# Kernel tuning notes

Hardware: AMD Instinct MI355X
Metric: run time of the kernel (lower is better)

The kernel has to match this reference:

```python
import jax, jax.numpy as jnp
import numpy as np

ATOM_K = 10
VOX_K = 15
HEADS = 4
HEAD_DIM = 32
N_BLOCKS = 4
BLOCK_DEPTH = 2


def _pairwise_sqdist(a, b):
    # a: [Na,3], b: [Nb,3] -> [Na,Nb]
    return jnp.sum(a * a, 1)[:, None] + jnp.sum(b * b, 1)[None, :] - 2.0 * (a @ b.T)


def knn(src_pos, dst_pos, k):
    # for each dst point, k nearest src points; returns (dst_idx, src_idx), each [Nd*k]
    d2 = _pairwise_sqdist(dst_pos, src_pos)
    _, idx = jax.lax.top_k(-d2, k)
    dst = jnp.repeat(jnp.arange(dst_pos.shape[0]), k)
    return dst, idx.reshape(-1)


def knn_graph(pos, k):
    # k nearest neighbors excluding self; returns (src=neighbor, dst=center)
    n = pos.shape[0]
    d2 = _pairwise_sqdist(pos, pos) + jnp.eye(n, dtype=pos.dtype) * 1e10
    _, idx = jax.lax.top_k(-d2, k)
    dst = jnp.repeat(jnp.arange(n), k)
    return idx.reshape(-1), dst


def edge_weights(i0, i1, h_a, pos_a, h_b, pos_b, w1, b1, w2, b2):
    # MLP([2*A+1, 8, 1]) on concat(h_a[i0], h_b[i1], dist) -> scalar per edge
    d = jnp.sqrt(jnp.sum((pos_a[i0] - pos_b[i1]) ** 2, -1, keepdims=True) + 1e-12)
    feat = jnp.concatenate([h_a[i0], h_b[i1], d], -1)
    return (jax.nn.relu(feat @ w1 + b1) @ w2 + b2)[:, 0]


def attn_layer(h, src, dst, ew, wq_l, wk_l, wv_l, n):
    # edge-weighted multi-head graph attention with segment softmax over dst
    q = (h @ wq_l).reshape(n, HEADS, HEAD_DIM)
    k = (h @ wk_l).reshape(n, HEADS, HEAD_DIM)
    v = (h @ wv_l).reshape(n, HEADS, HEAD_DIM)
    logits = jnp.sum(q[dst] * k[src], -1) / jnp.sqrt(jnp.float32(HEAD_DIM)) + ew[:, None]  # [E,H]
    m = jax.ops.segment_max(logits, dst, num_segments=n)
    z = jnp.exp(logits - m[dst])
    s = jax.ops.segment_sum(z, dst, num_segments=n)
    alpha = z / (s[dst] + 1e-9)
    out = jax.ops.segment_sum(alpha[:, :, None] * v[src], dst, num_segments=n)
    return out.reshape(n, HEADS * HEAD_DIM)


def layer_norm(x, g, b):
    mu = jnp.mean(x, -1, keepdims=True)
    var = jnp.var(x, -1, keepdims=True)
    return (x - mu) * jax.lax.rsqrt(var + 1e-5) * g + b


def setup_inputs() -> dict:
    Na, Nv, F, A, OUT = 8192, 4096, 64, 128, 128
    L = N_BLOCKS * BLOCK_DEPTH
    key = jax.random.key(0)
    ks = jax.random.split(key, 20)
    p = lambda k, shape, s=0.05: jax.random.normal(k, shape, jnp.float32) * s
    return {
        'atom_x': jax.random.normal(ks[0], (Na, F), jnp.float32),
        'atom_pos': jax.random.normal(ks[1], (Na, 3), jnp.float32) * 10.0,
        'vox_x': jax.random.normal(ks[2], (Nv, F), jnp.float32),
        'vox_pos': jax.random.normal(ks[3], (Nv, 3), jnp.float32) * 10.0,
        'w_atom_in': p(ks[4], (F, A)), 'b_atom_in': jnp.zeros((A,), jnp.float32),
        'w_vox_in': p(ks[5], (F, A)), 'b_vox_in': jnp.zeros((A,), jnp.float32),
        'aa_w1': p(ks[6], (2 * A + 1, 8)), 'aa_b1': jnp.zeros((8,), jnp.float32),
        'aa_w2': p(ks[7], (8, 1)), 'aa_b2': jnp.zeros((1,), jnp.float32),
        'av_w1': p(ks[8], (2 * A + 1, 8)), 'av_b1': jnp.zeros((8,), jnp.float32),
        'av_w2': p(ks[9], (8, 1)), 'av_b2': jnp.zeros((1,), jnp.float32),
        'vv_w1': p(ks[10], (2 * A + 1, 8)), 'vv_b1': jnp.zeros((8,), jnp.float32),
        'vv_w2': p(ks[11], (8, 1)), 'vv_b2': jnp.zeros((1,), jnp.float32),
        'wq': p(ks[12], (L, A, A)), 'wk': p(ks[13], (L, A, A)), 'wv': p(ks[14], (L, A, A)),
        'ln_g': jnp.ones((L, A), jnp.float32), 'ln_b': jnp.zeros((L, A), jnp.float32),
        'w_o1': p(ks[15], ((N_BLOCKS + 1) * A, A)), 'b_o1': jnp.zeros((A,), jnp.float32),
        'w_o2': p(ks[16], (A, OUT)), 'b_o2': jnp.zeros((OUT,), jnp.float32),
    }


def reference(atom_x, atom_pos, vox_x, vox_pos, w_atom_in, b_atom_in, w_vox_in, b_vox_in,
              aa_w1, aa_b1, aa_w2, aa_b2, av_w1, av_b1, av_w2, av_b2, vv_w1, vv_b1, vv_w2, vv_b2,
              wq, wk, wv, ln_g, ln_b, w_o1, b_o1, w_o2, b_o2):
    Na, Nv = atom_x.shape[0], vox_x.shape[0]
    N = Na + Nv
    atom_h0 = atom_x @ w_atom_in + b_atom_in
    vox_h0 = vox_x @ w_vox_in + b_vox_in

    # multi-scale KNN graph construction
    aa_src, aa_dst = knn_graph(atom_pos, ATOM_K)
    aa_ew = edge_weights(aa_src, aa_dst, atom_h0, atom_pos, atom_h0, atom_pos, aa_w1, aa_b1, aa_w2, aa_b2)
    av_vox, av_atom = knn(atom_pos, vox_pos, VOX_K)  # dst=vox, src=atom
    av_ew = edge_weights(av_vox, av_atom, vox_h0, vox_pos, atom_h0, atom_pos, av_w1, av_b1, av_w2, av_b2)
    vv_src, vv_dst = knn_graph(vox_pos, VOX_K)
    vv_ew = edge_weights(vv_src, vv_dst, vox_h0, vox_pos, vox_h0, vox_pos, vv_w1, vv_b1, vv_w2, vv_b2)

    # combined atom|vox graph (vox nodes offset by Na)
    src = jnp.concatenate([aa_src, av_atom, vv_src + Na])
    dst = jnp.concatenate([aa_dst, av_vox + Na, vv_dst + Na])
    ew = jnp.concatenate([aa_ew, av_ew, vv_ew])
    h = jnp.concatenate([atom_h0, vox_h0], 0)

    block_outs = []
    for b_i in range(N_BLOCKS):
        for l in range(BLOCK_DEPTH):
            li = b_i * BLOCK_DEPTH + l
            h = layer_norm(h + attn_layer(h, src, dst, ew, wq[li], wk[li], wv[li], N), ln_g[li], ln_b[li])
        block_outs.append(h[Na:])

    feat = jnp.concatenate([vox_h0] + block_outs, -1)  # [Nv, (blocks+1)*A]
    return jax.nn.relu(feat @ w_o1 + b_o1) @ w_o2 + b_o2
```

## Files before the change

kernel.cpp:

```cpp
#include <hip/hip_runtime.h>
#include <hip/hip_bf16.h>

#define PE_NA 8192
#define PE_NV 4096
#define PE_NN (PE_NA+PE_NV)
#define PE_FA 128
#define PE_FIN 64
#define PE_KAA 10
#define PE_KAV 15
#define PE_KVV 15
#define PE_EAA (PE_NA*PE_KAA)
#define PE_EAV (PE_NV*PE_KAV)
#define PE_EVV (PE_NV*PE_KVV)
#define PE_ETOT (PE_EAA+PE_EAV+PE_EVV)
#define PE_KNN_TILE 1024
#define PE_KNN_BLOCKS (PE_NA/4 + PE_NV/4 + PE_NV/4)
#define PE_P1A 0
#define PE_P2A 65536
#define PE_P2AV 131072
#define PE_P1AV 196608
#define PE_P1V 229376
#define PE_P2V 262144
#define PE_PTOT 294912
#define PE_PRE_BLOCKS (PE_PTOT/256)
#define PE_WT_ELEMS (8*3*128*128)
#define PE_WT_BLOCKS (PE_WT_ELEMS/256)

typedef __hip_bfloat16 bf16;
typedef __attribute__((ext_vector_type(4))) float f32x4;
typedef __attribute__((ext_vector_type(4))) unsigned int u32x4;
typedef __attribute__((ext_vector_type(8))) short s16x8;
union pe_frag { u32x4 u; s16x8 s; };

__device__ __forceinline__ float pe_b2f(bf16 x){ return __bfloat162float(x); }

__device__ __forceinline__ float pe_u2f(unsigned short u){ return __uint_as_float(((unsigned)u) << 16); }
__device__ __forceinline__ unsigned short pe_f2u(float f){
  unsigned u = __float_as_uint(f);
  u = u + 0x7FFFu + ((u >> 16) & 1u);
  return (unsigned short)(u >> 16);
}

__global__ __launch_bounds__(1024) void pe_probe_kernel(const unsigned short* __restrict__ buf, int n,
                                                        int* __restrict__ flag){
  __shared__ int red[16];
  int t = threadIdx.x;
  int cnt = 0;
  for (int i = t; i < n; i += 1024){
    unsigned u = buf[i];
    unsigned e = (u >> 7) & 0xFF;
    if (u == 0u || (e >= 100u && e <= 150u)) cnt++;
  }
  #pragma unroll
  for (int off = 32; off > 0; off >>= 1) cnt += __shfl_xor(cnt, off);
  if ((t & 63) == 0) red[t >> 6] = cnt;
  __syncthreads();
  if (t == 0){
    int s = 0;
    #pragma unroll
    for (int i = 0; i < 16; i++) s += red[i];
    flag[0] = (s > (n * 9) / 10) ? 0 : 1;
  }
}

struct PeConv {
  const void* src[29];
  long long dstOff[29];
  int n[29];
  int blk0[30];
};
__global__ __launch_bounds__(256) void pe_convall_kernel(PeConv a, float* __restrict__ wsbase,
                                                         const int* __restrict__ flag){
  int b = blockIdx.x;
  int s = 0;
  while (s < 28 && b >= a.blk0[s+1]) s++;
  int idx = (b - a.blk0[s])*256 + threadIdx.x;
  if (idx >= a.n[s]) return;
  float* dst = wsbase + a.dstOff[s];
  if (flag[0]) dst[idx] = ((const float*)a.src[s])[idx];
  else         dst[idx] = pe_b2f(((const bf16*)a.src[s])[idx]);
}

__global__ __launch_bounds__(256) void ProteinEncoder_558345749244_kernel(bf16* __restrict__ out, int n){
  int idx = blockIdx.x*256 + threadIdx.x;
  if (idx < n) out[idx] = __float2bfloat16(0.123f);
}

__global__ __launch_bounds__(256) void pe_packproj_kernel(
    const float* __restrict__ ax, const float* __restrict__ wai, const float* __restrict__ bai,
    const float* __restrict__ vx, const float* __restrict__ wvi, const float* __restrict__ bvi,
    const float* __restrict__ apos, const float* __restrict__ vpos,
    const float* __restrict__ wq, const float* __restrict__ wk, const float* __restrict__ wv,
    float* __restrict__ h, float* __restrict__ voxh0,
    float4* __restrict__ apos4, float4* __restrict__ vpos4,
    unsigned short* __restrict__ wtb){
  int b = blockIdx.x;
  const int NBA = (PE_NA*PE_FA)/256;
  const int NBV = (PE_NV*PE_FA)/256;
  const int NBP = (PE_NN + 255)/256;
  if (b < NBA){
    int idx = b*256 + threadIdx.x;
    int row = idx >> 7, col = idx & 127;
    const float* xr = ax + row*PE_FIN;
    float acc = bai[col];
    #pragma unroll 8
    for (int k2 = 0; k2 < PE_FIN; k2++) acc += xr[k2] * wai[k2*PE_FA + col];
    h[idx] = acc;
  } else if (b < NBA + NBV){
    int idx = (b - NBA)*256 + threadIdx.x;
    int row = idx >> 7, col = idx & 127;
    const float* xr = vx + row*PE_FIN;
    float acc = bvi[col];
    #pragma unroll 8
    for (int k2 = 0; k2 < PE_FIN; k2++) acc += xr[k2] * wvi[k2*PE_FA + col];
    h[(size_t)PE_NA*PE_FA + idx] = acc;
    voxh0[idx] = acc;
  } else if (b < NBA + NBV + NBP){
    int idx = (b - NBA - NBV)*256 + threadIdx.x;
    if (idx < PE_NA){
      float bx = apos[idx*3+0], by = apos[idx*3+1], bz = apos[idx*3+2];
      apos4[idx] = make_float4(bx, by, bz, (bx*bx + by*by) + bz*bz);
    } else if (idx < PE_NA + PE_NV){
      int j = idx - PE_NA;
      float bx = vpos[j*3+0], by = vpos[j*3+1], bz = vpos[j*3+2];
      vpos4[j] = make_float4(bx, by, bz, (bx*bx + by*by) + bz*bz);
    }
  } else {
    int g = (b - NBA - NBV - NBP)*256 + threadIdx.x;
    int c = g >> 14;
    int r = g & 16383;
    int n = r >> 7, k = r & 127;
    int li = c / 3, mat = c - li*3;
    const float* wsrc = (mat == 0) ? wq : (mat == 1) ? wk : wv;
    wtb[g] = pe_f2u(wsrc[li*16384 + k*128 + n]);
  }
}

__device__ __forceinline__ float pe_unflip(unsigned th){
  return __uint_as_float(th ^ ((unsigned)(~((int)th >> 31)) | 0x80000000u));
}
__device__ __forceinline__ void pe_knn_insert(unsigned long long mask, float d2, int j,
                                              int self, int K, int lane,
                                              unsigned long long &slot, float &thr_f){
  while (mask){
    int l = __ffsll((long long)mask) - 1;
    mask &= mask - 1;
    float dl = __shfl(d2, l, 64);
    int jl = __shfl(j, l, 64);
    if (jl == self) continue;
    unsigned u = __float_as_uint(dl);
    u ^= (unsigned)(((int)u >> 31) | 0x80000000);
    unsigned long long k = ((unsigned long long)u << 32) | (unsigned)jl;
    unsigned long long skm1 = __shfl(slot, K-1, 64);
    if (k < skm1){
      unsigned long long up = __shfl_up(slot, 1, 64);
      slot = (slot < k) ? slot : ((lane == 0 || up < k) ? k : up);
      thr_f = pe_unflip((unsigned)(__shfl(slot, K-1, 64) >> 32));
    }
  }
}

__global__ __launch_bounds__(256) void pe_knn3_kernel(const float4* __restrict__ apos4,
                                                      const float4* __restrict__ vpos4,
                                                      int* __restrict__ es,
                                                      const float* __restrict__ h,
                                                      const float* __restrict__ aw1,
                                                      const float* __restrict__ vw1,
                                                      const float* __restrict__ ww1,
                                                      float* __restrict__ Pall){
  __shared__ float4 s_tile[PE_KNN_TILE];
  int b = blockIdx.x;
  if (b >= PE_KNN_BLOCKS){
    int g = (b - PE_KNN_BLOCKS)*256 + threadIdx.x;
    const float* w1; const float* hb; int n; int half;
    if (g < PE_P2A)       { w1 = aw1; hb = h;                        n = g >> 3;               half = 0; }
    else if (g < PE_P2AV) { w1 = aw1; hb = h;                        n = (g - PE_P2A) >> 3;    half = 1; }
    else if (g < PE_P1AV) { w1 = vw1; hb = h;                        n = (g - PE_P2AV) >> 3;   half = 1; }
    else if (g < PE_P1V)  { w1 = vw1; hb = h + (size_t)PE_NA*PE_FA;  n = (g - PE_P1AV) >> 3;   half = 0; }
    else if (g < PE_P2V)  { w1 = ww1; hb = h + (size_t)PE_NA*PE_FA;  n = (g - PE_P1V) >> 3;    half = 0; }
    else                  { w1 = ww1; hb = h + (size_t)PE_NA*PE_FA;  n = (g - PE_P2V) >> 3;    half = 1; }
    int j = g & 7;
    const float* hr = hb + n*PE_FA;
    const float* wr = w1 + half*128*8 + j;
    float acc = 0.f;
    #pragma unroll 8
    for (int f = 0; f < 128; f++) acc += hr[f] * wr[f*8];
    Pall[g] = acc;
    return;
  }
  const float4 *dpos, *spos; int Ns, K, excl, idx_off, nb; int* out;
  if (b < PE_NA/4){
    dpos = apos4; spos = apos4; Ns = PE_NA; K = PE_KAA; excl = 1; idx_off = 0;
    out = es; nb = b;
  } else if (b < PE_NA/4 + PE_NV/4){
    dpos = vpos4; spos = apos4; Ns = PE_NA; K = PE_KAV; excl = 0; idx_off = 0;
    out = es + PE_EAA; nb = b - PE_NA/4;
  } else {
    dpos = vpos4; spos = vpos4; Ns = PE_NV; K = PE_KVV; excl = 1; idx_off = PE_NA;
    out = es + PE_EAA + PE_EAV; nb = b - PE_NA/4 - PE_NV/4;
  }
  int lane = threadIdx.x & 63;
  int n = nb*4 + (threadIdx.x >> 6);
  float4 dp = dpos[n];
  float ax = dp.x, ay = dp.y, az = dp.z;
  int self = excl ? n : -1;
  unsigned long long slot;
  float thr_f;
  {
    float4 pp = spos[lane];
    float dt = (ax*pp.x + ay*pp.y) + az*pp.z;
    float d2 = __builtin_fmaf(-2.0f, dt, pp.w);
    unsigned u = __float_as_uint(d2);
    u ^= (unsigned)(((int)u >> 31) | 0x80000000);
    if (excl && lane == n) u = 0xffffffffu;
    unsigned long long key = ((unsigned long long)u << 32) | (unsigned)lane;
    #pragma unroll
    for (int kk = 2; kk <= 64; kk <<= 1){
      #pragma unroll
      for (int jj = kk >> 1; jj > 0; jj >>= 1){
        unsigned long long o = __shfl_xor(key, jj, 64);
        bool keepmin = (((lane & jj) == 0) == ((lane & kk) == 0));
        unsigned long long mn = (key < o) ? key : o;
        unsigned long long mx = (key < o) ? o : key;
        key = keepmin ? mn : mx;
      }
    }
    slot = key;
    thr_f = pe_unflip((unsigned)(__shfl(slot, K-1, 64) >> 32));
  }
  for (int base = 0; base < Ns; base += PE_KNN_TILE){
    __syncthreads();
    #pragma unroll
    for (int i = 0; i < PE_KNN_TILE/256; i++)
      s_tile[i*256 + threadIdx.x] = spos[base + i*256 + threadIdx.x];
    __syncthreads();
    int c = (base == 0) ? (lane + 64) : lane;
    for (; c + 192 < PE_KNN_TILE; c += 256){
      float4 p0 = s_tile[c];
      float4 p1 = s_tile[c + 64];
      float4 p2 = s_tile[c + 128];
      float4 p3 = s_tile[c + 192];
      float dt0 = (ax*p0.x + ay*p0.y) + az*p0.z;
      float dt1 = (ax*p1.x + ay*p1.y) + az*p1.z;
      float dt2 = (ax*p2.x + ay*p2.y) + az*p2.z;
      float dt3 = (ax*p3.x + ay*p3.y) + az*p3.z;
      float d20 = __builtin_fmaf(-2.0f, dt0, p0.w);
      float d21 = __builtin_fmaf(-2.0f, dt1, p1.w);
      float d22 = __builtin_fmaf(-2.0f, dt2, p2.w);
      float d23 = __builtin_fmaf(-2.0f, dt3, p3.w);
      unsigned long long m0 = __ballot(d20 <= thr_f);
      unsigned long long m1 = __ballot(d21 <= thr_f);
      unsigned long long m2 = __ballot(d22 <= thr_f);
      unsigned long long m3 = __ballot(d23 <= thr_f);
      if (m0) pe_knn_insert(m0, d20, base + c,       self, K, lane, slot, thr_f);
      if (m1) pe_knn_insert(m1, d21, base + c + 64,  self, K, lane, slot, thr_f);
      if (m2) pe_knn_insert(m2, d22, base + c + 128, self, K, lane, slot, thr_f);
      if (m3) pe_knn_insert(m3, d23, base + c + 192, self, K, lane, slot, thr_f);
    }
    for (; c + 64 < PE_KNN_TILE; c += 128){
      float4 p0 = s_tile[c];
      float4 p1 = s_tile[c + 64];
      float dt0 = (ax*p0.x + ay*p0.y) + az*p0.z;
      float dt1 = (ax*p1.x + ay*p1.y) + az*p1.z;
      float d20 = __builtin_fmaf(-2.0f, dt0, p0.w);
      float d21 = __builtin_fmaf(-2.0f, dt1, p1.w);
      unsigned long long m0 = __ballot(d20 <= thr_f);
      unsigned long long m1 = __ballot(d21 <= thr_f);
      if (m0) pe_knn_insert(m0, d20, base + c,      self, K, lane, slot, thr_f);
      if (m1) pe_knn_insert(m1, d21, base + c + 64, self, K, lane, slot, thr_f);
    }
    if (c < PE_KNN_TILE){
      float4 p0 = s_tile[c];
      float dt0 = (ax*p0.x + ay*p0.y) + az*p0.z;
      float d20 = __builtin_fmaf(-2.0f, dt0, p0.w);
      unsigned long long m0 = __ballot(d20 <= thr_f);
      if (m0) pe_knn_insert(m0, d20, base + c, self, K, lane, slot, thr_f);
    }
  }
  if (lane < K) out[n*K + lane] = (int)(unsigned)(slot & 0xffffffffu) + idx_off;
}

__global__ __launch_bounds__(256) void pe_edge3_kernel(
    const float4* __restrict__ apos4, const float4* __restrict__ vpos4,
    const int* __restrict__ es, const float* __restrict__ Pall,
    const float* __restrict__ aw1, const float* __restrict__ ab1,
    const float* __restrict__ aw2, const float* __restrict__ ab2,
    const float* __restrict__ vw1, const float* __restrict__ vb1,
    const float* __restrict__ vw2, const float* __restrict__ vb2,
    const float* __restrict__ ww1, const float* __restrict__ wb1,
    const float* __restrict__ ww2, const float* __restrict__ wb2,
    float* __restrict__ ewb){
  int e = blockIdx.x*256 + threadIdx.x;
  const float *w1r, *b1, *w2, *b2;
  long long offA, offB;
  float4 qa, qb;
  if (e < PE_EAA){
    int dst = e / PE_KAA;
    int src = es[e];
    offA = PE_P1A  + (long long)src*8;
    offB = PE_P2A  + (long long)dst*8;
    qa = apos4[src]; qb = apos4[dst];
    w1r = aw1 + 256*8; b1 = ab1; w2 = aw2; b2 = ab2;
  } else if (e < PE_EAA + PE_EAV){
    int e2 = e - PE_EAA;
    int dstv = e2 / PE_KAV;
    int srca = es[e];
    offA = PE_P1AV + (long long)dstv*8;
    offB = PE_P2AV + (long long)srca*8;
    qa = vpos4[dstv]; qb = apos4[srca];
    w1r = vw1 + 256*8; b1 = vb1; w2 = vw2; b2 = vb2;
  } else {
    int e2 = e - PE_EAA - PE_EAV;
    int dstv = e2 / PE_KVV;
    int srcv = es[e] - PE_NA;
    offA = PE_P1V  + (long long)srcv*8;
    offB = PE_P2V  + (long long)dstv*8;
    qa = vpos4[srcv]; qb = vpos4[dstv];
    w1r = ww1 + 256*8; b1 = wb1; w2 = ww2; b2 = wb2;
  }
  float dx = qa.x - qb.x, dy = qa.y - qb.y, dz = qa.z - qb.z;
  float d = sqrtf(((dx*dx + dy*dy) + dz*dz) + 1e-12f);
  float4 a0 = *(const float4*)(Pall + offA);
  float4 a1 = *(const float4*)(Pall + offA + 4);
  float4 c0 = *(const float4*)(Pall + offB);
  float4 c1 = *(const float4*)(Pall + offB + 4);
  float acc[8] = { a0.x + c0.x, a0.y + c0.y, a0.z + c0.z, a0.w + c0.w,
                   a1.x + c1.x, a1.y + c1.y, a1.z + c1.z, a1.w + c1.w };
  float o = b2[0];
  #pragma unroll
  for (int j = 0; j < 8; j++){
    float hj = acc[j] + d*w1r[j] + b1[j];
    if (hj > 0.f) o += hj * w2[j];
  }
  ewb[e] = o;
}

__global__ __launch_bounds__(256) void pe_qkv3_kernel(const float* __restrict__ H,
    const unsigned short* __restrict__ Wt,
    unsigned short* __restrict__ QKV){
  __shared__ __align__(16) unsigned Xs[2048];
  int t = threadIdx.x;
  int row0 = blockIdx.x * 32;
  #pragma unroll
  for (int i = 0; i < 8; i++){
    int idx32 = i*256 + t;
    int row = idx32 >> 6, c32 = idx32 & 63;
    const float* src = H + (size_t)(row0 + row)*PE_FA + c32*2;
    unsigned u = (unsigned)pe_f2u(src[0]) | ((unsigned)pe_f2u(src[1]) << 16);
    Xs[row*64 + (c32 ^ ((row & 7) << 2))] = u;
  }
  __syncthreads();
  int w = t >> 6, l = t & 63;
  int l15 = l & 15, lq = l >> 4;
  f32x4 acc[2][6];
  #pragma unroll
  for (int a = 0; a < 2; a++)
    #pragma unroll
    for (int bb = 0; bb < 6; bb++) acc[a][bb] = (f32x4){0.f, 0.f, 0.f, 0.f};
  #pragma unroll
  for (int ks = 0; ks < 4; ks++){
    pe_frag af[2];
    #pragma unroll
    for (int rt = 0; rt < 2; rt++){
      int row = rt*16 + l15;
      int c32 = (ks*16 + lq*4) ^ ((row & 7) << 2);
      af[rt].u = *(const u32x4*)&Xs[row*64 + c32];
    }
    #pragma unroll
    for (int nt = 0; nt < 6; nt++){
      int n = w*96 + nt*16 + l15;
      pe_frag bf_;
      bf_.u = *(const u32x4*)(Wt + (size_t)n*PE_FA + ks*32 + lq*8);
      #pragma unroll
      for (int rt = 0; rt < 2; rt++)
        acc[rt][nt] = __builtin_amdgcn_mfma_f32_16x16x32_bf16(af[rt].s, bf_.s, acc[rt][nt], 0, 0, 0);
    }
  }
  #pragma unroll
  for (int rt = 0; rt < 2; rt++){
    #pragma unroll
    for (int nt = 0; nt < 6; nt++){
      int n = w*96 + nt*16 + l15;
      int mat = n >> 7, col = n & 127;
      unsigned short* outp = QKV + (size_t)mat*PE_NN*PE_FA + col;
      int nodeb = row0 + rt*16 + lq*4;
      #pragma unroll
      for (int v = 0; v < 4; v++)
        outp[(size_t)(nodeb + v)*PE_FA] = pe_f2u(acc[rt][nt][v]);
    }
  }
}

template<int DEG>
__device__ __forceinline__ void pe_attn_node(int n, int lane, int esel, float ewsel,
    const unsigned* __restrict__ Qp, const unsigned* __restrict__ Kp, const unsigned* __restrict__ Vp,
    float* H, const float* __restrict__ lng, const float* __restrict__ lnb, float* bout){
  unsigned qu = Qp[n*64 + lane];
  float qx = pe_u2f((unsigned short)(qu & 0xffffu));
  float qy = pe_u2f((unsigned short)(qu >> 16));
  int srcs[DEG];
  #pragma unroll
  for (int e = 0; e < DEG; e++) srcs[e] = __shfl(esel, e, 64);
  const float inv = 0.17677669529663687f;
  float lg[DEG];
  #pragma unroll
  for (int e = 0; e < DEG; e++){
    unsigned ku = Kp[srcs[e]*64 + lane];
    float p = qx*pe_u2f((unsigned short)(ku & 0xffffu)) + qy*pe_u2f((unsigned short)(ku >> 16));
    #pragma unroll
    for (int off = 8; off > 0; off >>= 1) p += __shfl_xor(p, off);
    lg[e] = p*inv + __shfl(ewsel, e, 64);
  }
  float m = -1e30f;
  #pragma unroll
  for (int e = 0; e < DEG; e++) m = fmaxf(m, lg[e]);
  float ssum = 0.f;
  #pragma unroll
  for (int e = 0; e < DEG; e++){ float z = expf(lg[e] - m); ssum += z; lg[e] = z; }
  float rdn = 1.0f / (ssum + 1e-9f);
  float a0 = 0.f, a1 = 0.f;
  #pragma unroll
  for (int e = 0; e < DEG; e++){
    unsigned vu = Vp[srcs[e]*64 + lane];
    a0 += lg[e]*pe_u2f((unsigned short)(vu & 0xffffu));
    a1 += lg[e]*pe_u2f((unsigned short)(vu >> 16));
  }
  a0 *= rdn; a1 *= rdn;
  float2 hv = ((const float2*)H)[n*64 + lane];
  float x0 = hv.x + a0, x1 = hv.y + a1;
  float s = x0 + x1;
  #pragma unroll
  for (int off = 32; off > 0; off >>= 1) s += __shfl_xor(s, off);
  float mu = s * (1.f/128.f);
  float d0 = x0 - mu, d1 = x1 - mu;
  float vq = d0*d0 + d1*d1;
  #pragma unroll
  for (int off = 32; off > 0; off >>= 1) vq += __shfl_xor(vq, off);
  float var = vq * (1.f/128.f);
  float rs = 1.0f / sqrtf(var + 1e-5f);
  float2 lw = ((const float2*)lng)[lane];
  float2 lb = ((const float2*)lnb)[lane];
  float2 yv = make_float2(d0*rs*lw.x + lb.x, d1*rs*lw.y + lb.y);
  ((float2*)H)[n*64 + lane] = yv;
  if (bout != nullptr) ((float2*)bout)[(n - PE_NA)*64 + lane] = yv;
}

__global__ __launch_bounds__(128) void pe_attn_ln_kernel(const unsigned* __restrict__ Qp,
    const unsigned* __restrict__ Kp, const unsigned* __restrict__ Vp, float* H,
    const int* __restrict__ esrc, const float* __restrict__ eew,
    const float* __restrict__ lng, const float* __restrict__ lnb, float* bout){
  int w = threadIdx.x >> 6;
  int lane = threadIdx.x & 63;
  int n = blockIdx.x*2 + w;
  int esel = 0; float ewsel = 0.f;
  if (n < PE_NA){
    if (lane < PE_KAA){ int e = n*PE_KAA + lane; esel = esrc[e]; ewsel = eew[e]; }
    pe_attn_node<PE_KAA>(n, lane, esel, ewsel, Qp, Kp, Vp, H, lng, lnb, nullptr);
  } else {
    int j = n - PE_NA;
    if (lane < PE_KAV){ int e = PE_EAA + j*PE_KAV + lane; esel = esrc[e]; ewsel = eew[e]; }
    else if (lane < PE_KAV + PE_KVV){ int e = PE_EAA + PE_EAV + j*PE_KVV + (lane - PE_KAV); esel = esrc[e]; ewsel = eew[e]; }
    pe_attn_node<PE_KAV+PE_KVV>(n, lane, esel, ewsel, Qp, Kp, Vp, H, lng, lnb, bout);
  }
}

__global__ __launch_bounds__(256) void pe_final1_kernel(const float* __restrict__ voxh0, const float* __restrict__ bouts,
    const float* __restrict__ W, const float* __restrict__ B, float* __restrict__ hid){
  __shared__ float Xs[640][17];
  int t = threadIdx.x;
  int row0 = blockIdx.x * 16;
  for (int s = 0; s < 5; s++){
    const float* seg = (s == 0) ? voxh0 : (bouts + (size_t)(s-1)*PE_NV*PE_FA);
    #pragma unroll
    for (int i = 0; i < 8; i++){
      int idx = i*256 + t;
      int r = idx >> 7, k0 = idx & 127;
      Xs[s*128 + k0][r] = seg[(size_t)(row0 + r)*PE_FA + k0];
    }
  }
  __syncthreads();
  int col = t & 127;
  int rg = (t >> 7) * 8;
  float acc[8];
  #pragma unroll
  for (int i = 0; i < 8; i++) acc[i] = B[col];
  for (int k = 0; k < 640; k++){
    float w = W[k*PE_FA + col];
    #pragma unroll
    for (int i = 0; i < 8; i++) acc[i] += Xs[k][rg + i] * w;
  }
  #pragma unroll
  for (int i = 0; i < 8; i++)
    hid[(size_t)(row0 + rg + i)*PE_FA + col] = fmaxf(acc[i], 0.f);
}

__global__ __launch_bounds__(256) void pe_final2_kernel(const float* __restrict__ hid, const float* __restrict__ W,
    const float* __restrict__ B, void* __restrict__ outv, const int* __restrict__ flag){
  int idx = blockIdx.x*256 + threadIdx.x;
  int r = idx >> 7, c = idx & 127;
  float acc = B[c];
  const float* hr = hid + r*PE_FA;
  #pragma unroll 8
  for (int k2 = 0; k2 < 128; k2++) acc += hr[k2] * W[k2*PE_FA + c];
  if (flag[0]) ((float*)outv)[idx] = acc;
  else         ((bf16*)outv)[idx] = __float2bfloat16(acc);
}

extern "C" void kernel_launch(void* const* d_in, const int* in_sizes, int n_in,
                              void* d_out, int out_size, void* d_ws, size_t ws_size,
                              hipStream_t stream){
  (void)in_sizes; (void)n_in; (void)ws_size;

  float* ws = (float*)d_ws;
  int* flag = (int*)ws;
  float* p = ws + 4;
  auto A = [&](size_t n){ float* r = p; p += n; return r; };

  float* c_atom_x  = A(PE_NA*PE_FIN);
  float* c_atom_pos= A(PE_NA*3);
  float* c_vox_x   = A(PE_NV*PE_FIN);
  float* c_vox_pos = A(PE_NV*3);
  float* c_w_ai = A(PE_FIN*PE_FA); float* c_b_ai = A(PE_FA);
  float* c_w_vi = A(PE_FIN*PE_FA); float* c_b_vi = A(PE_FA);
  float* c_aa_w1 = A(257*8); float* c_aa_b1 = A(8); float* c_aa_w2 = A(8); float* c_aa_b2 = A(1);
  float* c_av_w1 = A(257*8); float* c_av_b1 = A(8); float* c_av_w2 = A(8); float* c_av_b2 = A(1);
  float* c_vv_w1 = A(257*8); float* c_vv_b1 = A(8); float* c_vv_w2 = A(8); float* c_vv_b2 = A(1);
  float* c_wq = A(8*PE_FA*PE_FA); float* c_wk = A(8*PE_FA*PE_FA); float* c_wv = A(8*PE_FA*PE_FA);
  float* c_lng = A(8*PE_FA); float* c_lnb = A(8*PE_FA);
  float* c_wo1 = A(5*PE_FA*PE_FA); float* c_bo1 = A(PE_FA);
  float* c_wo2 = A(PE_FA*PE_FA);   float* c_bo2 = A(PE_FA);

  float* h     = A((size_t)PE_NN*PE_FA);
  float* voxh0 = A((size_t)PE_NV*PE_FA);
  int*   es    = (int*)A(PE_ETOT);
  float* ewb   = A(PE_ETOT);
  float* bouts = A((size_t)4*PE_NV*PE_FA);
  float4* apos4 = (float4*)A((size_t)PE_NA*4);
  float4* vpos4 = (float4*)A((size_t)PE_NV*4);
  { uintptr_t up = (uintptr_t)p; up = (up + 15) & ~(uintptr_t)15; p = (float*)up; }
  float* Pall  = A(PE_PTOT);
  unsigned short* wtb = (unsigned short*)A(PE_WT_ELEMS/2);
  float* qkvb  = A((size_t)3*PE_NN*64);
  unsigned short* qkvb16 = (unsigned short*)qkvb;
  float* hid   = qkvb;

  pe_probe_kernel<<<1, 1024, 0, stream>>>((const unsigned short*)d_in[1], PE_NA*3, flag);

  const int nelem[29] = {
    PE_NA*PE_FIN, PE_NA*3, PE_NV*PE_FIN, PE_NV*3,
    PE_FIN*PE_FA, PE_FA, PE_FIN*PE_FA, PE_FA,
    257*8, 8, 8, 1,  257*8, 8, 8, 1,  257*8, 8, 8, 1,
    8*PE_FA*PE_FA, 8*PE_FA*PE_FA, 8*PE_FA*PE_FA,
    8*PE_FA, 8*PE_FA,
    5*PE_FA*PE_FA, PE_FA, PE_FA*PE_FA, PE_FA
  };
  float* cdst[29] = {
    c_atom_x, c_atom_pos, c_vox_x, c_vox_pos,
    c_w_ai, c_b_ai, c_w_vi, c_b_vi,
    c_aa_w1, c_aa_b1, c_aa_w2, c_aa_b2,
    c_av_w1, c_av_b1, c_av_w2, c_av_b2,
    c_vv_w1, c_vv_b1, c_vv_w2, c_vv_b2,
    c_wq, c_wk, c_wv, c_lng, c_lnb,
    c_wo1, c_bo1, c_wo2, c_bo2
  };
  PeConv pc;
  int bacc = 0;
  for (int i = 0; i < 29; i++){
    pc.src[i] = d_in[i];
    pc.n[i] = nelem[i];
    pc.dstOff[i] = (long long)(cdst[i] - ws);
    pc.blk0[i] = bacc;
    bacc += (nelem[i] + 255)/256;
  }
  pc.blk0[29] = bacc;
  pe_convall_kernel<<<bacc, 256, 0, stream>>>(pc, ws, flag);

  ProteinEncoder_558345749244_kernel<<<(out_size + 255)/256, 256, 0, stream>>>((bf16*)d_out, out_size);

  pe_packproj_kernel<<<(PE_NA*PE_FA)/256 + (PE_NV*PE_FA)/256 + (PE_NN + 255)/256 + PE_WT_BLOCKS,
                       256, 0, stream>>>(
      c_atom_x, c_w_ai, c_b_ai, c_vox_x, c_w_vi, c_b_vi, c_atom_pos, c_vox_pos,
      c_wq, c_wk, c_wv,
      h, voxh0, apos4, vpos4, wtb);

  pe_knn3_kernel<<<PE_KNN_BLOCKS + PE_PRE_BLOCKS, 256, 0, stream>>>(
      apos4, vpos4, es, h, c_aa_w1, c_av_w1, c_vv_w1, Pall);

  pe_edge3_kernel<<<PE_ETOT/256, 256, 0, stream>>>(
      apos4, vpos4, es, Pall,
      c_aa_w1, c_aa_b1, c_aa_w2, c_aa_b2,
      c_av_w1, c_av_b1, c_av_w2, c_av_b2,
      c_vv_w1, c_vv_b1, c_vv_w2, c_vv_b2,
      ewb);

  const unsigned* Qp = (const unsigned*)qkvb;
  const unsigned* Kp = Qp + (size_t)PE_NN*64;
  const unsigned* Vp = Kp + (size_t)PE_NN*64;
  for (int li = 0; li < 8; li++){
    pe_qkv3_kernel<<<PE_NN/32, 256, 0, stream>>>(h, wtb + (size_t)li*3*PE_FA*PE_FA, qkvb16);
    float* bo = (li & 1) ? (bouts + (size_t)(li >> 1)*PE_NV*PE_FA) : nullptr;
    pe_attn_ln_kernel<<<PE_NN/2, 128, 0, stream>>>(Qp, Kp, Vp,
                                                   h, es, ewb, c_lng + li*PE_FA, c_lnb + li*PE_FA, bo);
  }

  pe_final1_kernel<<<PE_NV/16, 256, 0, stream>>>(voxh0, bouts, c_wo1, c_bo1, hid);
  pe_final2_kernel<<<(PE_NV*PE_FA)/256, 256, 0, stream>>>(hid, c_wo2, c_bo2, d_out, flag);
}
```

Measured before the change: 627.3 us.

## Replace brute-force KNN scan with x-sorted sweep and early termination

Adds a single-block bitonic sort of atom and voxel positions by x coordinate. The KNN kernel then starts from each query's rank, found either from a stored rank or a two-level ballot search, and expands left and right in 64-point chunks. It stops once the x gap squared exceeds the current k-th distance, so it no longer scans all source points per query. This adds a serialized sort kernel launched on only two blocks plus uncoalesced global loads in place of shared-memory tiles. Tie handling can differ because keys now use original indices in a different scan order.

```diff
diff --git a/kernel.cpp b/kernel.cpp
--- a/kernel.cpp
+++ b/kernel.cpp
@@ -13,7 +13,6 @@
 #define PE_EAV (PE_NV*PE_KAV)
 #define PE_EVV (PE_NV*PE_KVV)
 #define PE_ETOT (PE_EAA+PE_EAV+PE_EVV)
-#define PE_KNN_TILE 1024
 #define PE_KNN_BLOCKS (PE_NA/4 + PE_NV/4 + PE_NV/4)
 #define PE_P1A 0
 #define PE_P2A 65536
@@ -136,18 +135,56 @@
   }
 }
 
+__global__ __launch_bounds__(1024) void pe_sortx_kernel(
+    const float4* __restrict__ apos4, const float4* __restrict__ vpos4,
+    float4* __restrict__ sax4, int* __restrict__ said, int* __restrict__ arank,
+    float4* __restrict__ svx4, int* __restrict__ svid, int* __restrict__ vrank){
+  __shared__ unsigned long long keys[PE_NA];
+  int N = (blockIdx.x == 0) ? PE_NA : PE_NV;
+  const float4* src = (blockIdx.x == 0) ? apos4 : vpos4;
+  float4* d4  = (blockIdx.x == 0) ? sax4 : svx4;
+  int* did    = (blockIdx.x == 0) ? said : svid;
+  int* drk    = (blockIdx.x == 0) ? arank : vrank;
+  int t = threadIdx.x;
+  for (int i = t; i < N; i += 1024){
+    unsigned u = __float_as_uint(src[i].x);
+    u ^= (unsigned)(((int)u >> 31) | 0x80000000);
+    keys[i] = ((unsigned long long)u << 32) | (unsigned)i;
+  }
+  __syncthreads();
+  for (int k = 2; k <= N; k <<= 1){
+    for (int j = k >> 1; j > 0; j >>= 1){
+      for (int i = t; i < N; i += 1024){
+        int ip = i ^ j;
+        if (ip > i){
+          bool asc = ((i & k) == 0);
+          unsigned long long a = keys[i], c = keys[ip];
+          if ((a > c) == asc){ keys[i] = c; keys[ip] = a; }
+        }
+      }
+      __syncthreads();
+    }
+  }
+  for (int i = t; i < N; i += 1024){
+    unsigned long long kk = keys[i];
+    int oi = (int)(unsigned)(kk & 0xffffffffu);
+    d4[i] = src[oi];
+    did[i] = oi;
+    drk[oi] = i;
+  }
+}
+
 __device__ __forceinline__ float pe_unflip(unsigned th){
   return __uint_as_float(th ^ ((unsigned)(~((int)th >> 31)) | 0x80000000u));
 }
 __device__ __forceinline__ void pe_knn_insert(unsigned long long mask, float d2, int j,
-                                              int self, int K, int lane,
+                                              int K, int lane,
                                               unsigned long long &slot, float &thr_f){
   while (mask){
     int l = __ffsll((long long)mask) - 1;
     mask &= mask - 1;
     float dl = __shfl(d2, l, 64);
     int jl = __shfl(j, l, 64);
-    if (jl == self) continue;
     unsigned u = __float_as_uint(dl);
     u ^= (unsigned)(((int)u >> 31) | 0x80000000);
     unsigned long long k = ((unsigned long long)u << 32) | (unsigned)jl;
@@ -160,15 +197,14 @@
   }
 }
 
-__global__ __launch_bounds__(256) void pe_knn3_kernel(const float4* __restrict__ apos4,
-                                                      const float4* __restrict__ vpos4,
-                                                      int* __restrict__ es,
-                                                      const float* __restrict__ h,
-                                                      const float* __restrict__ aw1,
-                                                      const float* __restrict__ vw1,
-                                                      const float* __restrict__ ww1,
-                                                      float* __restrict__ Pall){
-  __shared__ float4 s_tile[PE_KNN_TILE];
+__global__ __launch_bounds__(256) void pe_knn3_kernel(
+    const float4* __restrict__ apos4, const float4* __restrict__ vpos4,
+    const float4* __restrict__ sax4, const int* __restrict__ said, const int* __restrict__ arank,
+    const float4* __restrict__ svx4, const int* __restrict__ svid, const int* __restrict__ vrank,
+    int* __restrict__ es,
+    const float* __restrict__ h,
+    const float* __restrict__ aw1, const float* __restrict__ vw1, const float* __restrict__ ww1,
+    float* __restrict__ Pall){
   int b = blockIdx.x;
   if (b >= PE_KNN_BLOCKS){
     int g = (b - PE_KNN_BLOCKS)*256 + threadIdx.x;
@@ -188,32 +224,55 @@
     Pall[g] = acc;
     return;
   }
-  const float4 *dpos, *spos; int Ns, K, excl, idx_off, nb; int* out;
+  const float4 *dpos, *spos; const int *sid, *srank; int Ns, K, excl, idx_off, nb; int* out;
   if (b < PE_NA/4){
-    dpos = apos4; spos = apos4; Ns = PE_NA; K = PE_KAA; excl = 1; idx_off = 0;
-    out = es; nb = b;
+    dpos = apos4; spos = sax4; sid = said; srank = arank;
+    Ns = PE_NA; K = PE_KAA; excl = 1; idx_off = 0; out = es; nb = b;
   } else if (b < PE_NA/4 + PE_NV/4){
-    dpos = vpos4; spos = apos4; Ns = PE_NA; K = PE_KAV; excl = 0; idx_off = 0;
-    out = es + PE_EAA; nb = b - PE_NA/4;
+    dpos = vpos4; spos = sax4; sid = said; srank = nullptr;
+    Ns = PE_NA; K = PE_KAV; excl = 0; idx_off = 0; out = es + PE_EAA; nb = b - PE_NA/4;
   } else {
-    dpos = vpos4; spos = vpos4; Ns = PE_NV; K = PE_KVV; excl = 1; idx_off = PE_NA;
+    dpos = vpos4; spos = svx4; sid = svid; srank = vrank;
+    Ns = PE_NV; K = PE_KVV; excl = 1; idx_off = PE_NA;
     out = es + PE_EAA + PE_EAV; nb = b - PE_NA/4 - PE_NV/4;
   }
   int lane = threadIdx.x & 63;
   int n = nb*4 + (threadIdx.x >> 6);
   float4 dp = dpos[n];
-  float ax = dp.x, ay = dp.y, az = dp.z;
+  float qx = dp.x, qy = dp.y, qz = dp.z, nq = dp.w;
   int self = excl ? n : -1;
+  int start;
+  if (srank){
+    start = srank[n];
+  } else {
+    int lo = 0, len = Ns;
+    #pragma unroll
+    for (int it = 0; it < 2; it++){
+      int step = (len + 63) >> 6;
+      int pr = lo + lane*step; if (pr > Ns-1) pr = Ns-1;
+      float px = spos[pr].x;
+      unsigned long long mv = __ballot(px <= qx);
+      int cnt = __popcll(mv);
+      int seg = cnt > 0 ? cnt - 1 : 0;
+      lo = lo + seg*step;
+      len = step;
+      if (lo > Ns-1) lo = Ns-1;
+    }
+    start = lo;
+  }
+  int w0 = start - 32; if (w0 < 0) w0 = 0; if (w0 > Ns - 64) w0 = Ns - 64;
   unsigned long long slot;
   float thr_f;
   {
-    float4 pp = spos[lane];
-    float dt = (ax*pp.x + ay*pp.y) + az*pp.z;
-    float d2 = __builtin_fmaf(-2.0f, dt, pp.w);
+    int j = w0 + lane;
+    float4 pp = spos[j];
+    int oi = sid[j];
+    float dt = (qx*pp.x + qy*pp.y) + qz*pp.z;
+    float d2 = __builtin_fmaf(-2.0f, dt, nq + pp.w);
     unsigned u = __float_as_uint(d2);
     u ^= (unsigned)(((int)u >> 31) | 0x80000000);
-    if (excl && lane == n) u = 0xffffffffu;
-    unsigned long long key = ((unsigned long long)u << 32) | (unsigned)lane;
+    if (oi == self) u = 0xffffffffu;
+    unsigned long long key = ((unsigned long long)u << 32) | (unsigned)oi;
     #pragma unroll
     for (int kk = 2; kk <= 64; kk <<= 1){
       #pragma unroll
@@ -228,53 +287,43 @@
     slot = key;
     thr_f = pe_unflip((unsigned)(__shfl(slot, K-1, 64) >> 32));
   }
-  for (int base = 0; base < Ns; base += PE_KNN_TILE){
-    __syncthreads();
-    #pragma unroll
-    for (int i = 0; i < PE_KNN_TILE/256; i++)
-      s_tile[i*256 + threadIdx.x] = spos[base + i*256 + threadIdx.x];
-    __syncthreads();
-    int c = (base == 0) ? (lane + 64) : lane;
-    for (; c + 192 < PE_KNN_TILE; c += 256){
-      float4 p0 = s_tile[c];
-      float4 p1 = s_tile[c + 64];
-      float4 p2 = s_tile[c + 128];
-      float4 p3 = s_tile[c + 192];
-      float dt0 = (ax*p0.x + ay*p0.y) + az*p0.z;
-      float dt1 = (ax*p1.x + ay*p1.y) + az*p1.z;
-      float dt2 = (ax*p2.x + ay*p2.y) + az*p2.z;
-      float dt3 = (ax*p3.x + ay*p3.y) + az*p3.z;
-      float d20 = __builtin_fmaf(-2.0f, dt0, p0.w);
-      float d21 = __builtin_fmaf(-2.0f, dt1, p1.w);
-      float d22 = __builtin_fmaf(-2.0f, dt2, p2.w);
-      float d23 = __builtin_fmaf(-2.0f, dt3, p3.w);
-      unsigned long long m0 = __ballot(d20 <= thr_f);
-      unsigned long long m1 = __ballot(d21 <= thr_f);
-      unsigned long long m2 = __ballot(d22 <= thr_f);
-      unsigned long long m3 = __ballot(d23 <= thr_f);
-      if (m0) pe_knn_insert(m0, d20, base + c,       self, K, lane, slot, thr_f);
-      if (m1) pe_knn_insert(m1, d21, base + c + 64,  self, K, lane, slot, thr_f);
-      if (m2) pe_knn_insert(m2, d22, base + c + 128, self, K, lane, slot, thr_f);
-      if (m3) pe_knn_insert(m3, d23, base + c + 192, self, K, lane, slot, thr_f);
-    }
-    for (; c + 64 < PE_KNN_TILE; c += 128){
-      float4 p0 = s_tile[c];
-      float4 p1 = s_tile[c + 64];
-      float dt0 = (ax*p0.x + ay*p0.y) + az*p0.z;
-      float dt1 = (ax*p1.x + ay*p1.y) + az*p1.z;
-      float d20 = __builtin_fmaf(-2.0f, dt0, p0.w);
-      float d21 = __builtin_fmaf(-2.0f, dt1, p1.w);
-      unsigned long long m0 = __ballot(d20 <= thr_f);
-      unsigned long long m1 = __ballot(d21 <= thr_f);
-      if (m0) pe_knn_insert(m0, d20, base + c,      self, K, lane, slot, thr_f);
-      if (m1) pe_knn_insert(m1, d21, base + c + 64, self, K, lane, slot, thr_f);
-    }
-    if (c < PE_KNN_TILE){
-      float4 p0 = s_tile[c];
-      float dt0 = (ax*p0.x + ay*p0.y) + az*p0.z;
-      float d20 = __builtin_fmaf(-2.0f, dt0, p0.w);
-      unsigned long long m0 = __ballot(d20 <= thr_f);
-      if (m0) pe_knn_insert(m0, d20, base + c, self, K, lane, slot, thr_f);
+  int L = w0 - 1;
+  int R = w0 + 64;
+  bool doneL = false, doneR = false;
+  while (!(doneL && doneR)){
+    if (!doneL){
+      int j = L - lane;
+      bool val = (j >= 0);
+      float d2 = 1e30f, ddx = -1e30f; int oi = -3;
+      if (val){
+        float4 pp = spos[j];
+        oi = sid[j];
+        ddx = pp.x - qx;
+        float dt = (qx*pp.x + qy*pp.y) + qz*pp.z;
+        d2 = __builtin_fmaf(-2.0f, dt, nq + pp.w);
+      }
+      unsigned long long m = __ballot(val && (d2 <= thr_f) && (oi != self));
+      if (m) pe_knn_insert(m, d2, oi, K, lane, slot, thr_f);
+      float dd63 = __shfl(ddx, 63);
+      doneL = (L - 64 < 0) || ((dd63 < 0.f) && (dd63*dd63 > thr_f));
+      L -= 64;
+    }
+    if (!doneR){
+      int j = R + lane;
+      bool val = (j < Ns);
+      float d2 = 1e30f, ddx = 1e30f; int oi = -3;
+      if (val){
+        float4 pp = spos[j];
+        oi = sid[j];
+        ddx = pp.x - qx;
+        float dt = (qx*pp.x + qy*pp.y) + qz*pp.z;
+        d2 = __builtin_fmaf(-2.0f, dt, nq + pp.w);
+      }
+      unsigned long long m = __ballot(val && (d2 <= thr_f) && (oi != self));
+      if (m) pe_knn_insert(m, d2, oi, K, lane, slot, thr_f);
+      float dd63 = __shfl(ddx, 63);
+      doneR = (R + 64 >= Ns) || ((dd63 > 0.f) && (dd63*dd63 > thr_f));
+      R += 64;
     }
   }
   if (lane < K) out[n*K + lane] = (int)(unsigned)(slot & 0xffffffffu) + idx_off;
@@ -537,6 +586,12 @@
   float* bouts = A((size_t)4*PE_NV*PE_FA);
   float4* apos4 = (float4*)A((size_t)PE_NA*4);
   float4* vpos4 = (float4*)A((size_t)PE_NV*4);
+  float4* sax4  = (float4*)A((size_t)PE_NA*4);
+  float4* svx4  = (float4*)A((size_t)PE_NV*4);
+  int* said  = (int*)A(PE_NA);
+  int* arank = (int*)A(PE_NA);
+  int* svid  = (int*)A(PE_NV);
+  int* vrank = (int*)A(PE_NV);
   { uintptr_t up = (uintptr_t)p; up = (up + 15) & ~(uintptr_t)15; p = (float*)up; }
   float* Pall  = A(PE_PTOT);
   unsigned short* wtb = (unsigned short*)A(PE_WT_ELEMS/2);
@@ -583,8 +638,11 @@
       c_wq, c_wk, c_wv,
       h, voxh0, apos4, vpos4, wtb);
 
+  pe_sortx_kernel<<<2, 1024, 0, stream>>>(apos4, vpos4, sax4, said, arank, svx4, svid, vrank);
+
   pe_knn3_kernel<<<PE_KNN_BLOCKS + PE_PRE_BLOCKS, 256, 0, stream>>>(
-      apos4, vpos4, es, h, c_aa_w1, c_av_w1, c_vv_w1, Pall);
+      apos4, vpos4, sax4, said, arank, svx4, svid, vrank,
+      es, h, c_aa_w1, c_av_w1, c_vv_w1, Pall);
 
   pe_edge3_kernel<<<PE_ETOT/256, 256, 0, stream>>>(
       apos4, vpos4, es, Pall,
```

Measured after the change: 695.9 us. +10.9%, slower.
